# Kernel optimization log

Measured on AMD Instinct MI355X. Metric: run time of the kernel, lower is better.

## Reference

```python
import jax, jax.numpy as jnp
import numpy as np

NEG = -9e15
ALPHA = 0.2  # leaky-relu slope


def gat_layer(h, mask, W, a, concat):
    # h: [N, Fin], W: [Fin, Fout], a: [2*Fout, 1], mask: [N, N]
    Wh = h @ W                                   # [N, Fout]
    F = Wh.shape[1]
    e = jax.nn.leaky_relu(Wh @ a[:F] + (Wh @ a[F:]).T, ALPHA)  # [N, N]
    att = jax.nn.softmax(jnp.where(mask > 0, e, NEG), axis=1)
    out = att @ Wh                               # [N, Fout]
    return jax.nn.elu(out) if concat else out


def gat(x, mask, W, a, Wo, ao):
    # W: [H, Fin, Fhid], a: [H, 2*Fhid, 1]
    heads = jax.vmap(lambda Wi, ai: gat_layer(x, mask, Wi, ai, True))(W, a)  # [H, N, Fhid]
    h = jnp.transpose(heads, (1, 0, 2)).reshape(x.shape[0], -1)  # [N, H*Fhid] (concat dim=1)
    return jax.nn.elu(gat_layer(h, mask, Wo, ao, False))


def setup_inputs() -> dict:
    key = jax.random.key(0)
    ks = jax.random.split(key, 16)
    N, Fin, H, Fhid, Ffin, P = 4096, 256, 4, 64, 64, 16
    x = jax.random.normal(ks[0], (N, Fin), jnp.float32)
    eye = jnp.eye(N, dtype=jnp.float32)
    sadj = jnp.maximum((jax.random.uniform(ks[1], (N, N)) < 0.005).astype(jnp.float32), eye)
    sadj2 = jnp.maximum((jax.random.uniform(ks[2], (N, N)) < 0.005).astype(jnp.float32), eye)
    s = 0.1
    inp = {
        "x": x, "sadj": sadj, "sadj2": sadj2,
        "W1": s * jax.random.normal(ks[3], (H, Fin, Fhid), jnp.float32),
        "a1": s * jax.random.normal(ks[4], (H, 2 * Fhid, 1), jnp.float32),
        "Wo1": s * jax.random.normal(ks[5], (H * Fhid, Ffin), jnp.float32),
        "ao1": s * jax.random.normal(ks[6], (2 * Ffin, 1), jnp.float32),
        "W2": s * jax.random.normal(ks[7], (H, Fin, Fhid), jnp.float32),
        "a2": s * jax.random.normal(ks[8], (H, 2 * Fhid, 1), jnp.float32),
        "Wo2": s * jax.random.normal(ks[9], (H * Fhid, Ffin), jnp.float32),
        "ao2": s * jax.random.normal(ks[10], (2 * Ffin, 1), jnp.float32),
        "Wp1": s * jax.random.normal(ks[11], (Ffin, P), jnp.float32),
        "bp1": jnp.zeros((P,), jnp.float32),
        "Wp2": s * jax.random.normal(ks[12], (P, 1), jnp.float32),
    }
    return inp


def reference(x, sadj, sadj2, W1, a1, Wo1, ao1, W2, a2, Wo2, ao2, Wp1, bp1, Wp2):
    emb1 = gat(x, sadj, W1, a1, Wo1, ao1)    # [N, Ffin]
    emb2 = gat(x, sadj2, W2, a2, Wo2, ao2)   # [N, Ffin]
    emb = jnp.stack([emb1, emb2], axis=1)    # [N, 2, Ffin]
    w = jnp.tanh(emb @ Wp1 + bp1) @ Wp2      # [N, 2, 1]
    beta = jax.nn.softmax(w, axis=1)
    return jnp.sum(beta * emb, axis=1)       # [N, Ffin]
```

## Files before the change

### kernel.cpp

```cpp
#include <hip/hip_runtime.h>
#include <hip/hip_bf16.h>
#include <stdint.h>


typedef short short8 __attribute__((ext_vector_type(8)));
typedef __bf16 bf16x8 __attribute__((ext_vector_type(8)));
typedef float floatx4 __attribute__((ext_vector_type(4)));
typedef unsigned int uintx4 __attribute__((ext_vector_type(4)));

#define MAXDEG 128
#define LRELU 0.2f

template <typename V>
__device__ inline auto mfma_impl(V a, V b, floatx4 c, int)
    -> decltype(__builtin_amdgcn_mfma_f32_16x16x32_bf16(a, b, c, 0, 0, 0)) {
  return __builtin_amdgcn_mfma_f32_16x16x32_bf16(a, b, c, 0, 0, 0);
}
template <typename V>
__device__ inline floatx4 mfma_impl(V a, V b, floatx4 c, long) {
  return __builtin_amdgcn_mfma_f32_16x16x32_bf16(
      __builtin_bit_cast(bf16x8, a), __builtin_bit_cast(bf16x8, b), c, 0, 0, 0);
}
__device__ inline floatx4 MFMA16(short8 a, short8 b, floatx4 c) {
  return mfma_impl(a, b, c, 0);
}

__device__ inline bool is_bf16_inputs(const void* sadj) {
  return ((*(const uint32_t*)sadj) & 0xFFFFu) == 0x3F80u;
}
__device__ inline float ldval(const void* p, size_t i, bool isbf) {
  if (isbf) return __bfloat162float(((const __hip_bfloat16*)p)[i]);
  return ((const float*)p)[i];
}
__device__ inline uint16_t f2bf_bits(float f) {
  __hip_bfloat16 h = __float2bfloat16(f);
  return *(uint16_t*)&h;
}

static constexpr size_t OFF_ADJ = 0;
static constexpr size_t OFF_DEG = OFF_ADJ + (size_t)2 * 4096 * MAXDEG * 4;
static constexpr size_t OFF_XB  = OFF_DEG + (size_t)2 * 4096 * 4;
static constexpr size_t OFF_WT  = OFF_XB  + (size_t)4096 * 256 * 2;
static constexpr size_t OFF_WOT = OFF_WT  + (size_t)2 * 4 * 64 * 256 * 2;
static constexpr size_t OFF_AV  = OFF_WOT + (size_t)2 * 64 * 256 * 2;
static constexpr size_t OFF_AOV = OFF_AV  + (size_t)2 * 4 * 128 * 4;
static constexpr size_t OFF_WP1 = OFF_AOV + (size_t)2 * 128 * 4;
static constexpr size_t OFF_BP1 = OFF_WP1 + (size_t)64 * 16 * 4;
static constexpr size_t OFF_WP2 = OFF_BP1 + 64;
static constexpr size_t OFF_WH1 = OFF_WP2 + 192;
static constexpr size_t OFF_S1  = OFF_WH1 + (size_t)2 * 4096 * 256 * 4;
static constexpr size_t OFF_D1  = OFF_S1  + (size_t)2 * 4 * 4096 * 4;
static constexpr size_t OFF_H2  = OFF_D1  + (size_t)2 * 4 * 4096 * 4;
static constexpr size_t OFF_WH2 = OFF_H2  + (size_t)2 * 4096 * 256 * 2;
static constexpr size_t OFF_S2  = OFF_WH2 + (size_t)2 * 4096 * 64 * 4;
static constexpr size_t OFF_D2  = OFF_S2  + (size_t)2 * 4096 * 4;
static constexpr size_t OFF_EMB = OFF_D2  + (size_t)2 * 4096 * 4;
static constexpr size_t OFF_MB  = OFF_EMB + (size_t)2 * 4096 * 64 * 4;

__global__ __launch_bounds__(256) void k_conv(const void* x,
    const void* W1, const void* W2, const void* Wo1, const void* Wo2,
    const void* a1, const void* a2, const void* ao1, const void* ao2,
    const void* wp1, const void* bp1, const void* wp2, const void* sadj,
    uint16_t* xb, uint16_t* Wt, uint16_t* Wot,
    float* Av, float* Aov, float* Wp1v, float* Bp1v, float* Wp2v) {
  bool isbf = is_bf16_inputs(sadj);
  int bid = blockIdx.x;
  if (bid < 1024) {
    int i0 = (bid * 256 + threadIdx.x) * 4;
    if (isbf) {
      *(uint64_t*)(xb + i0) = *(const uint64_t*)((const uint16_t*)x + i0);
    } else {
      const float* xf = (const float*)x;
      float4 f = *(const float4*)(xf + i0);
      xb[i0 + 0] = f2bf_bits(f.x);
      xb[i0 + 1] = f2bf_bits(f.y);
      xb[i0 + 2] = f2bf_bits(f.z);
      xb[i0 + 3] = f2bf_bits(f.w);
    }
    return;
  }
  int idx = (bid - 1024) * 256 + threadIdx.x;
  if (idx < 131072) {
    int k = idx & 255, f = (idx >> 8) & 63, h = (idx >> 14) & 3, g = idx >> 16;
    const void* W = g ? W2 : W1;
    Wt[idx] = f2bf_bits(ldval(W, (size_t)h * 16384 + (size_t)k * 64 + f, isbf));
  } else if (idx < 163840) {
    int j = idx - 131072;
    int k = j & 255, f = (j >> 8) & 63, g = j >> 14;
    const void* W = g ? Wo2 : Wo1;
    Wot[j] = f2bf_bits(ldval(W, (size_t)k * 64 + f, isbf));
  } else if (idx < 166176) {
    int q = idx - 163840;
    if (q < 512)        Av[q] = ldval(a1, q, isbf);
    else if (q < 1024)  Av[q] = ldval(a2, q - 512, isbf);
    else if (q < 1152)  Aov[q - 1024] = ldval(ao1, q - 1024, isbf);
    else if (q < 1280)  Aov[q - 1152 + 128] = ldval(ao2, q - 1152, isbf);
    else if (q < 2304)  Wp1v[q - 1280] = ldval(wp1, q - 1280, isbf);
    else if (q < 2320)  Bp1v[q - 2304] = ldval(bp1, q - 2304, isbf);
    else                Wp2v[q - 2320] = ldval(wp2, q - 2320, isbf);
  }
}

__global__ __launch_bounds__(256) void k_scan(const void* sadj, const void* sadj2,
                                              uint8_t* mbytes) {
  bool isbf = is_bf16_inputs(sadj);
  int tid = blockIdx.x * blockDim.x + threadIdx.x;
  int nt = gridDim.x * blockDim.x;
  const int NCHUNK = 4194304;
  if (isbf) {
    const uint16_t* m0 = (const uint16_t*)sadj;
    const uint16_t* m1 = (const uint16_t*)sadj2;
    for (int c = tid; c < NCHUNK; c += nt) {
      const uint16_t* src = (c < 2097152) ? m0 : m1;
      int cc = c & 2097151;
      uintx4 v = __builtin_nontemporal_load((const uintx4*)src + cc);
      uint32_t wd[4] = {v.x, v.y, v.z, v.w};
      uint32_t byte = 0;
#pragma unroll
      for (int k = 0; k < 8; ++k) {
        uint16_t val = (uint16_t)(wd[k >> 1] >> ((k & 1) * 16));
        if (val != 0 && !(val & 0x8000)) byte |= 1u << k;
      }
      mbytes[c] = (uint8_t)byte;
    }
  } else {
    const float* m0 = (const float*)sadj;
    const float* m1 = (const float*)sadj2;
    for (int c = tid; c < NCHUNK; c += nt) {
      const float* src = (c < 2097152) ? m0 : m1;
      size_t cc = (size_t)(c & 2097151) * 8;
      floatx4 va = __builtin_nontemporal_load((const floatx4*)(src + cc));
      floatx4 vb = __builtin_nontemporal_load((const floatx4*)(src + cc + 4));
      float vals[8] = {va.x, va.y, va.z, va.w, vb.x, vb.y, vb.z, vb.w};
      uint32_t byte = 0;
#pragma unroll
      for (int k = 0; k < 8; ++k)
        if (vals[k] > 0.f) byte |= 1u << k;
      mbytes[c] = (uint8_t)byte;
    }
  }
}

__global__ __launch_bounds__(256) void k_compact(const uint8_t* mbytes,
                                                 int* adj, int* deg) {
  int w = blockIdx.x * 4 + (threadIdx.x >> 6);
  int lane = threadIdx.x & 63;
  uint64_t bits = *((const uint64_t*)(mbytes + (size_t)w * 512) + lane);
  int* out = adj + (size_t)w * MAXDEG;
  int c = __popcll(bits);
  int pre = c;
#pragma unroll
  for (int o = 1; o < 64; o <<= 1) {
    int tv = __shfl_up(pre, o);
    if (lane >= o) pre += tv;
  }
  int total = __shfl(pre, 63);
  int off = pre - c;
  int base = lane * 64;
  while (bits) {
    int i = __ffsll((unsigned long long)bits) - 1;
    bits &= bits - 1;
    if (off < MAXDEG) out[off] = base + i;
    ++off;
  }
  if (lane == 0) deg[w] = total < MAXDEG ? total : MAXDEG;
}

__global__ __launch_bounds__(256) void k_gemm1(const uint16_t* xb, const uint16_t* Wt,
                                               const float* Av,
                                               float* Wh1, float* s1, float* d1) {
  int w = blockIdx.x * 4 + (threadIdx.x >> 6);
  int lane = threadIdx.x & 63;
  int q = lane >> 4, c = lane & 15;
  int g = w >> 10, rem = w & 1023;
  int m0 = (rem >> 2) << 4, h = rem & 3;
  const uint16_t* B = Wt + (size_t)(g * 4 + h) * 64 * 256;
  floatx4 acc[4] = {};
  const uint16_t* arow = xb + (size_t)(m0 + c) * 256 + q * 8;
  for (int kk = 0; kk < 8; ++kk) {
    short8 a = *(const short8*)(arow + kk * 32);
#pragma unroll
    for (int t = 0; t < 4; ++t) {
      short8 b = *(const short8*)(B + (size_t)(t * 16 + c) * 256 + kk * 32 + q * 8);
      acc[t] = MFMA16(a, b, acc[t]);
    }
  }
  float* Crow = Wh1 + (size_t)(g * 4096 + m0) * 256 + h * 64;
#pragma unroll
  for (int t = 0; t < 4; ++t)
#pragma unroll
    for (int r = 0; r < 4; ++r)
      Crow[(size_t)(q * 4 + r) * 256 + t * 16 + c] = acc[t][r];
  const float* ag = Av + (g * 4 + h) * 128;
  float as[4], ad[4];
#pragma unroll
  for (int t = 0; t < 4; ++t) { as[t] = ag[t * 16 + c]; ad[t] = ag[64 + t * 16 + c]; }
#pragma unroll
  for (int r = 0; r < 4; ++r) {
    float ps = 0.f, pd = 0.f;
#pragma unroll
    for (int t = 0; t < 4; ++t) { ps += acc[t][r] * as[t]; pd += acc[t][r] * ad[t]; }
#pragma unroll
    for (int o = 1; o < 16; o <<= 1) { ps += __shfl_xor(ps, o); pd += __shfl_xor(pd, o); }
    if (c == 0) {
      int n = m0 + q * 4 + r;
      s1[((size_t)(g * 4096 + n)) * 4 + h] = ps;
      d1[((size_t)(g * 4096 + n)) * 4 + h] = pd;
    }
  }
}

__global__ __launch_bounds__(256) void k_gemm2(const uint16_t* h2, const uint16_t* Wot,
                                               const float* Aov,
                                               float* Wh2, float* s2, float* d2) {
  int w = blockIdx.x * 4 + (threadIdx.x >> 6);
  int lane = threadIdx.x & 63;
  int q = lane >> 4, c = lane & 15;
  int g = w >> 8, m0 = (w & 255) << 4;
  const uint16_t* A = h2 + (size_t)g * 4096 * 256;
  const uint16_t* B = Wot + (size_t)g * 64 * 256;
  floatx4 acc[4] = {};
  const uint16_t* arow = A + (size_t)(m0 + c) * 256 + q * 8;
  for (int kk = 0; kk < 8; ++kk) {
    short8 a = *(const short8*)(arow + kk * 32);
#pragma unroll
    for (int t = 0; t < 4; ++t) {
      short8 b = *(const short8*)(B + (size_t)(t * 16 + c) * 256 + kk * 32 + q * 8);
      acc[t] = MFMA16(a, b, acc[t]);
    }
  }
  float* Crow = Wh2 + (size_t)(g * 4096 + m0) * 64;
#pragma unroll
  for (int t = 0; t < 4; ++t)
#pragma unroll
    for (int r = 0; r < 4; ++r)
      Crow[(size_t)(q * 4 + r) * 64 + t * 16 + c] = acc[t][r];
  const float* ag = Aov + g * 128;
  float as[4], ad[4];
#pragma unroll
  for (int t = 0; t < 4; ++t) { as[t] = ag[t * 16 + c]; ad[t] = ag[64 + t * 16 + c]; }
#pragma unroll
  for (int r = 0; r < 4; ++r) {
    float ps = 0.f, pd = 0.f;
#pragma unroll
    for (int t = 0; t < 4; ++t) { ps += acc[t][r] * as[t]; pd += acc[t][r] * ad[t]; }
#pragma unroll
    for (int o = 1; o < 16; o <<= 1) { ps += __shfl_xor(ps, o); pd += __shfl_xor(pd, o); }
    if (c == 0) {
      int n = m0 + q * 4 + r;
      s2[g * 4096 + n] = ps;
      d2[g * 4096 + n] = pd;
    }
  }
}

__global__ __launch_bounds__(256) void k_att1(const int* adj, const int* deg,
    const float* s1, const float* d1, const float* Wh1, uint16_t* h2) {
  __shared__ float pbuf[4][4][MAXDEG];
  __shared__ int jbuf[4][MAXDEG];
  int wv = threadIdx.x >> 6, lane = threadIdx.x & 63;
  int w = blockIdx.x * 4 + wv;
  int g = w >> 12;
  int gn = w;
  int dg = deg[gn];
  const int* nbr = adj + (size_t)gn * MAXDEG;
  float4 s4 = *(const float4*)(s1 + (size_t)gn * 4);
  const float4* d4 = (const float4*)(d1) + (size_t)g * 4096;

  bool v0 = lane < dg, v1 = lane + 64 < dg;
  int j0 = 0, j1 = 0;
  if (v0) j0 = nbr[lane];
  if (v1) j1 = nbr[lane + 64];
  float4 dj0 = d4[j0];
  float4 dj1 = d4[j1];
  if (v0) jbuf[wv][lane] = j0;
  if (v1) jbuf[wv][lane + 64] = j1;

  const float ninf = -3.0e38f;
  float sa[4] = {s4.x, s4.y, s4.z, s4.w};
  float d0a[4] = {dj0.x, dj0.y, dj0.z, dj0.w};
  float d1a[4] = {dj1.x, dj1.y, dj1.z, dj1.w};
#pragma unroll
  for (int h = 0; h < 4; ++h) {
    float t0 = sa[h] + d0a[h]; t0 = t0 > 0.f ? t0 : LRELU * t0;
    float t1 = sa[h] + d1a[h]; t1 = t1 > 0.f ? t1 : LRELU * t1;
    float e0 = v0 ? t0 : ninf;
    float e1 = v1 ? t1 : ninf;
    float m = fmaxf(e0, e1);
#pragma unroll
    for (int o = 32; o; o >>= 1) m = fmaxf(m, __shfl_xor(m, o));
    float p0 = v0 ? __expf(e0 - m) : 0.f;
    float p1 = v1 ? __expf(e1 - m) : 0.f;
    float l = p0 + p1;
#pragma unroll
    for (int o = 32; o; o >>= 1) l += __shfl_xor(l, o);
    float inv = __frcp_rn(l);
    pbuf[wv][h][lane] = p0 * inv;
    pbuf[wv][h][lane + 64] = p1 * inv;
  }
  int myh = lane >> 4;
  const float* prow = pbuf[wv][myh];
  const int* jb = jbuf[wv];
  const float4* Wg = (const float4*)(Wh1) + (size_t)g * 4096 * 64;
  float ax = 0.f, ay = 0.f, az = 0.f, aw = 0.f;
  for (int i = 0; i < dg; i += 8) {
    float pv[8];
    float4 wv8[8];
#pragma unroll
    for (int k = 0; k < 8; ++k) {
      int idx = i + k;
      bool vv = idx < dg;
      int sidx = vv ? idx : 0;
      int j = jb[sidx];
      pv[k] = vv ? prow[sidx] : 0.f;
      wv8[k] = Wg[(size_t)j * 64 + lane];
    }
#pragma unroll
    for (int k = 0; k < 8; ++k) {
      ax += pv[k] * wv8[k].x;
      ay += pv[k] * wv8[k].y;
      az += pv[k] * wv8[k].z;
      aw += pv[k] * wv8[k].w;
    }
  }
  ax = ax > 0.f ? ax : __expf(ax) - 1.f;
  ay = ay > 0.f ? ay : __expf(ay) - 1.f;
  az = az > 0.f ? az : __expf(az) - 1.f;
  aw = aw > 0.f ? aw : __expf(aw) - 1.f;
  ushort4 o4 = {f2bf_bits(ax), f2bf_bits(ay), f2bf_bits(az), f2bf_bits(aw)};
  *(ushort4*)(h2 + (size_t)gn * 256 + lane * 4) = o4;
}

__global__ __launch_bounds__(256) void k_att2(const int* adj, const int* deg,
    const float* s2, const float* d2, const float* Wh2, float* emb) {
  __shared__ float pbuf[4][MAXDEG];
  __shared__ int jbuf[4][MAXDEG];
  int wv = threadIdx.x >> 6, lane = threadIdx.x & 63;
  int w = blockIdx.x * 4 + wv;
  int g = w >> 12;
  int gn = w;
  int dg = deg[gn];
  const int* nbr = adj + (size_t)gn * MAXDEG;
  float sn = s2[gn];
  const float* dp = d2 + (size_t)g * 4096;

  bool v0 = lane < dg, v1 = lane + 64 < dg;
  int j0 = 0, j1 = 0;
  if (v0) j0 = nbr[lane];
  if (v1) j1 = nbr[lane + 64];
  float dd0 = dp[j0], dd1 = dp[j1];
  if (v0) jbuf[wv][lane] = j0;
  if (v1) jbuf[wv][lane + 64] = j1;

  const float ninf = -3.0e38f;
  float t0 = sn + dd0; t0 = t0 > 0.f ? t0 : LRELU * t0;
  float t1 = sn + dd1; t1 = t1 > 0.f ? t1 : LRELU * t1;
  float e0 = v0 ? t0 : ninf;
  float e1 = v1 ? t1 : ninf;
  float m = fmaxf(e0, e1);
#pragma unroll
  for (int o = 32; o; o >>= 1) m = fmaxf(m, __shfl_xor(m, o));
  float p0 = v0 ? __expf(e0 - m) : 0.f;
  float p1 = v1 ? __expf(e1 - m) : 0.f;
  float l = p0 + p1;
#pragma unroll
  for (int o = 32; o; o >>= 1) l += __shfl_xor(l, o);
  float inv = __frcp_rn(l);
  pbuf[wv][lane] = p0 * inv;
  pbuf[wv][lane + 64] = p1 * inv;

  int mye = lane >> 4, c4 = lane & 15;
  const float4* Wg = (const float4*)(Wh2) + (size_t)g * 4096 * 16;
  float ax = 0.f, ay = 0.f, az = 0.f, aw = 0.f;
  for (int i = 0; i < dg; i += 8) {
    int ia = i + mye, ib = i + 4 + mye;
    bool va = ia < dg, vb = ib < dg;
    int sa_ = va ? ia : 0, sb_ = vb ? ib : 0;
    int ja = jbuf[wv][sa_], jb2 = jbuf[wv][sb_];
    float pa = va ? pbuf[wv][sa_] : 0.f;
    float pb = vb ? pbuf[wv][sb_] : 0.f;
    float4 wa = Wg[(size_t)ja * 16 + c4];
    float4 wb = Wg[(size_t)jb2 * 16 + c4];
    ax += pa * wa.x + pb * wb.x;
    ay += pa * wa.y + pb * wb.y;
    az += pa * wa.z + pb * wb.z;
    aw += pa * wa.w + pb * wb.w;
  }
#pragma unroll
  for (int o = 16; o <= 32; o <<= 1) {
    ax += __shfl_xor(ax, o);
    ay += __shfl_xor(ay, o);
    az += __shfl_xor(az, o);
    aw += __shfl_xor(aw, o);
  }
  if (lane < 16) {
    ax = ax > 0.f ? ax : __expf(ax) - 1.f;
    ay = ay > 0.f ? ay : __expf(ay) - 1.f;
    az = az > 0.f ? az : __expf(az) - 1.f;
    aw = aw > 0.f ? aw : __expf(aw) - 1.f;
    float4 r = {ax, ay, az, aw};
    *(float4*)(emb + (size_t)gn * 64 + lane * 4) = r;
  }
}

__global__ __launch_bounds__(256) void k_final(const float* emb, const float* Wp1v,
    const float* Bp1v, const float* Wp2v, const void* sadj, void* out) {
  __shared__ float se[4][128];
  __shared__ float st[4][32];
  __shared__ float sw[4][2];
  int wv = threadIdx.x >> 6, lane = threadIdx.x & 63;
  int n = blockIdx.x * 4 + wv;
  bool isbf = is_bf16_inputs(sadj);
  float e1 = emb[(size_t)n * 64 + lane];
  float e2 = emb[(size_t)(4096 + n) * 64 + lane];
  se[wv][lane] = e1;
  se[wv][64 + lane] = e2;
  __syncthreads();
  if (lane < 32) {
    int g = lane >> 4, p = lane & 15;
    float s = Bp1v[p];
    const float* eb = &se[wv][g * 64];
    for (int f = 0; f < 64; ++f) s += eb[f] * Wp1v[f * 16 + p];
    st[wv][lane] = tanhf(s);
  }
  __syncthreads();
  if (lane < 2) {
    float s = 0.f;
    for (int p = 0; p < 16; ++p) s += st[wv][lane * 16 + p] * Wp2v[p];
    sw[wv][lane] = s;
  }
  __syncthreads();
  float w0 = sw[wv][0], w1 = sw[wv][1];
  float mx = fmaxf(w0, w1);
  float p0 = __expf(w0 - mx), p1 = __expf(w1 - mx);
  float inv = 1.f / (p0 + p1);
  float v = (p0 * e1 + p1 * e2) * inv;
  if (isbf) ((uint16_t*)out)[(size_t)n * 64 + lane] = f2bf_bits(v);
  else ((float*)out)[(size_t)n * 64 + lane] = v;
}

extern "C" void kernel_launch(void* const* d_in, const int* in_sizes, int n_in,
                              void* d_out, int out_size, void* d_ws, size_t ws_size,
                              hipStream_t stream) {
  const void* x    = d_in[0];
  const void* sadj = d_in[1];
  const void* sadj2 = d_in[2];
  const void* W1  = d_in[3];
  const void* a1  = d_in[4];
  const void* Wo1 = d_in[5];
  const void* ao1 = d_in[6];
  const void* W2  = d_in[7];
  const void* a2  = d_in[8];
  const void* Wo2 = d_in[9];
  const void* ao2 = d_in[10];
  const void* Wp1 = d_in[11];
  const void* bp1 = d_in[12];
  const void* Wp2 = d_in[13];

  char* ws = (char*)d_ws;
  int* adj      = (int*)(ws + OFF_ADJ);
  int* deg      = (int*)(ws + OFF_DEG);
  uint16_t* xb  = (uint16_t*)(ws + OFF_XB);
  uint16_t* Wt  = (uint16_t*)(ws + OFF_WT);
  uint16_t* Wot = (uint16_t*)(ws + OFF_WOT);
  float* Av     = (float*)(ws + OFF_AV);
  float* Aov    = (float*)(ws + OFF_AOV);
  float* Wp1v   = (float*)(ws + OFF_WP1);
  float* Bp1v   = (float*)(ws + OFF_BP1);
  float* Wp2v   = (float*)(ws + OFF_WP2);
  float* Wh1    = (float*)(ws + OFF_WH1);
  float* s1     = (float*)(ws + OFF_S1);
  float* d1     = (float*)(ws + OFF_D1);
  uint16_t* h2  = (uint16_t*)(ws + OFF_H2);
  float* Wh2    = (float*)(ws + OFF_WH2);
  float* s2     = (float*)(ws + OFF_S2);
  float* d2     = (float*)(ws + OFF_D2);
  float* emb    = (float*)(ws + OFF_EMB);
  uint8_t* mb   = (uint8_t*)(ws + OFF_MB);

  k_scan<<<1024, 256, 0, stream>>>(sadj, sadj2, mb);
  k_conv<<<1680, 256, 0, stream>>>(x, W1, W2, Wo1, Wo2, a1, a2, ao1, ao2,
                                   Wp1, bp1, Wp2, sadj,
                                   xb, Wt, Wot, Av, Aov, Wp1v, Bp1v, Wp2v);
  k_compact<<<2048, 256, 0, stream>>>(mb, adj, deg);
  k_gemm1<<<512, 256, 0, stream>>>(xb, Wt, Av, Wh1, s1, d1);
  k_att1<<<2048, 256, 0, stream>>>(adj, deg, s1, d1, Wh1, h2);
  k_gemm2<<<128, 256, 0, stream>>>(h2, Wot, Aov, Wh2, s2, d2);
  k_att2<<<2048, 256, 0, stream>>>(adj, deg, s2, d2, Wh2, emb);
  k_final<<<1024, 256, 0, stream>>>(emb, Wp1v, Bp1v, Wp2v, sadj, d_out);
}
```

Baseline: 225.1 us.

## Merge scan/conv and compact/gemm1 kernels, store Wh in bf16, fuse final into att2

Combines the mask scan with input conversion, and the adjacency compaction with the first GEMM, so that independent work shares a launch and eight kernels drop to five. The intermediate Wh1 and Wh2 projections are now stored in bf16 instead of fp32, which halves the bytes moved by the neighbour gathers in the attention kernels. The semantic-attention combine is fused into att2, so per-node embeddings stay in shared memory and are never written to global memory. The mask scan also switches from nontemporal loads to plain loads. The trade-off is extra bf16 rounding of Wh and larger kernels with more divergent block roles.

```diff
diff --git a/kernel.cpp b/kernel.cpp
--- a/kernel.cpp
+++ b/kernel.cpp
@@ -35,6 +35,10 @@
 __device__ inline uint16_t f2bf_bits(float f) {
   __hip_bfloat16 h = __float2bfloat16(f);
   return *(uint16_t*)&h;
+}
+__device__ inline float bf2f(uint16_t u) {
+  uint32_t i = ((uint32_t)u) << 16;
+  return __builtin_bit_cast(float, i);
 }
 
 static constexpr size_t OFF_ADJ = 0;
@@ -47,26 +51,64 @@
 static constexpr size_t OFF_WP1 = OFF_AOV + (size_t)2 * 128 * 4;
 static constexpr size_t OFF_BP1 = OFF_WP1 + (size_t)64 * 16 * 4;
 static constexpr size_t OFF_WP2 = OFF_BP1 + 64;
-static constexpr size_t OFF_WH1 = OFF_WP2 + 192;
-static constexpr size_t OFF_S1  = OFF_WH1 + (size_t)2 * 4096 * 256 * 4;
+static constexpr size_t OFF_WH1B = OFF_WP2 + 192;
+static constexpr size_t OFF_S1  = OFF_WH1B + (size_t)2 * 4096 * 256 * 2;
 static constexpr size_t OFF_D1  = OFF_S1  + (size_t)2 * 4 * 4096 * 4;
 static constexpr size_t OFF_H2  = OFF_D1  + (size_t)2 * 4 * 4096 * 4;
-static constexpr size_t OFF_WH2 = OFF_H2  + (size_t)2 * 4096 * 256 * 2;
-static constexpr size_t OFF_S2  = OFF_WH2 + (size_t)2 * 4096 * 64 * 4;
+static constexpr size_t OFF_WH2B = OFF_H2 + (size_t)2 * 4096 * 256 * 2;
+static constexpr size_t OFF_S2  = OFF_WH2B + (size_t)2 * 4096 * 64 * 2;
 static constexpr size_t OFF_D2  = OFF_S2  + (size_t)2 * 4096 * 4;
-static constexpr size_t OFF_EMB = OFF_D2  + (size_t)2 * 4096 * 4;
-static constexpr size_t OFF_MB  = OFF_EMB + (size_t)2 * 4096 * 64 * 4;
-
-__global__ __launch_bounds__(256) void k_conv(const void* x,
+static constexpr size_t OFF_MB  = OFF_D2  + (size_t)2 * 4096 * 4;
+
+__global__ __launch_bounds__(256) void k_pre(const void* sadj, const void* sadj2,
+    const void* x,
     const void* W1, const void* W2, const void* Wo1, const void* Wo2,
     const void* a1, const void* a2, const void* ao1, const void* ao2,
-    const void* wp1, const void* bp1, const void* wp2, const void* sadj,
-    uint16_t* xb, uint16_t* Wt, uint16_t* Wot,
+    const void* wp1, const void* bp1, const void* wp2,
+    uint8_t* mbytes, uint16_t* xb, uint16_t* Wt, uint16_t* Wot,
     float* Av, float* Aov, float* Wp1v, float* Bp1v, float* Wp2v) {
   bool isbf = is_bf16_inputs(sadj);
   int bid = blockIdx.x;
-  if (bid < 1024) {
-    int i0 = (bid * 256 + threadIdx.x) * 4;
+  if (bid < 2048) {
+    int tid = bid * 256 + threadIdx.x;
+    int nt = 2048 * 256;
+    const int NCHUNK = 4194304;
+    if (isbf) {
+      const uint16_t* m0 = (const uint16_t*)sadj;
+      const uint16_t* m1 = (const uint16_t*)sadj2;
+      for (int c = tid; c < NCHUNK; c += nt) {
+        const uint16_t* src = (c < 2097152) ? m0 : m1;
+        int cc = c & 2097151;
+        uintx4 v = *((const uintx4*)src + cc);
+        uint32_t wd[4] = {v.x, v.y, v.z, v.w};
+        uint32_t byte = 0;
+#pragma unroll
+        for (int k = 0; k < 8; ++k) {
+          uint16_t val = (uint16_t)(wd[k >> 1] >> ((k & 1) * 16));
+          if (val != 0 && !(val & 0x8000)) byte |= 1u << k;
+        }
+        mbytes[c] = (uint8_t)byte;
+      }
+    } else {
+      const float* m0 = (const float*)sadj;
+      const float* m1 = (const float*)sadj2;
+      for (int c = tid; c < NCHUNK; c += nt) {
+        const float* src = (c < 2097152) ? m0 : m1;
+        size_t cc = (size_t)(c & 2097151) * 8;
+        floatx4 va = *(const floatx4*)(src + cc);
+        floatx4 vb = *(const floatx4*)(src + cc + 4);
+        float vals[8] = {va.x, va.y, va.z, va.w, vb.x, vb.y, vb.z, vb.w};
+        uint32_t byte = 0;
+#pragma unroll
+        for (int k = 0; k < 8; ++k)
+          if (vals[k] > 0.f) byte |= 1u << k;
+        mbytes[c] = (uint8_t)byte;
+      }
+    }
+    return;
+  }
+  if (bid < 3072) {
+    int i0 = ((bid - 2048) * 256 + threadIdx.x) * 4;
     if (isbf) {
       *(uint64_t*)(xb + i0) = *(const uint64_t*)((const uint16_t*)x + i0);
     } else {
@@ -79,7 +121,7 @@
     }
     return;
   }
-  int idx = (bid - 1024) * 256 + threadIdx.x;
+  int idx = (bid - 3072) * 256 + threadIdx.x;
   if (idx < 131072) {
     int k = idx & 255, f = (idx >> 8) & 63, h = (idx >> 14) & 3, g = idx >> 16;
     const void* W = g ? W2 : W1;
@@ -101,75 +143,35 @@
   }
 }
 
-__global__ __launch_bounds__(256) void k_scan(const void* sadj, const void* sadj2,
-                                              uint8_t* mbytes) {
-  bool isbf = is_bf16_inputs(sadj);
-  int tid = blockIdx.x * blockDim.x + threadIdx.x;
-  int nt = gridDim.x * blockDim.x;
-  const int NCHUNK = 4194304;
-  if (isbf) {
-    const uint16_t* m0 = (const uint16_t*)sadj;
-    const uint16_t* m1 = (const uint16_t*)sadj2;
-    for (int c = tid; c < NCHUNK; c += nt) {
-      const uint16_t* src = (c < 2097152) ? m0 : m1;
-      int cc = c & 2097151;
-      uintx4 v = __builtin_nontemporal_load((const uintx4*)src + cc);
-      uint32_t wd[4] = {v.x, v.y, v.z, v.w};
-      uint32_t byte = 0;
-#pragma unroll
-      for (int k = 0; k < 8; ++k) {
-        uint16_t val = (uint16_t)(wd[k >> 1] >> ((k & 1) * 16));
-        if (val != 0 && !(val & 0x8000)) byte |= 1u << k;
-      }
-      mbytes[c] = (uint8_t)byte;
-    }
-  } else {
-    const float* m0 = (const float*)sadj;
-    const float* m1 = (const float*)sadj2;
-    for (int c = tid; c < NCHUNK; c += nt) {
-      const float* src = (c < 2097152) ? m0 : m1;
-      size_t cc = (size_t)(c & 2097151) * 8;
-      floatx4 va = __builtin_nontemporal_load((const floatx4*)(src + cc));
-      floatx4 vb = __builtin_nontemporal_load((const floatx4*)(src + cc + 4));
-      float vals[8] = {va.x, va.y, va.z, va.w, vb.x, vb.y, vb.z, vb.w};
-      uint32_t byte = 0;
-#pragma unroll
-      for (int k = 0; k < 8; ++k)
-        if (vals[k] > 0.f) byte |= 1u << k;
-      mbytes[c] = (uint8_t)byte;
-    }
-  }
-}
-
-__global__ __launch_bounds__(256) void k_compact(const uint8_t* mbytes,
-                                                 int* adj, int* deg) {
-  int w = blockIdx.x * 4 + (threadIdx.x >> 6);
-  int lane = threadIdx.x & 63;
-  uint64_t bits = *((const uint64_t*)(mbytes + (size_t)w * 512) + lane);
-  int* out = adj + (size_t)w * MAXDEG;
-  int c = __popcll(bits);
-  int pre = c;
-#pragma unroll
-  for (int o = 1; o < 64; o <<= 1) {
-    int tv = __shfl_up(pre, o);
-    if (lane >= o) pre += tv;
-  }
-  int total = __shfl(pre, 63);
-  int off = pre - c;
-  int base = lane * 64;
-  while (bits) {
-    int i = __ffsll((unsigned long long)bits) - 1;
-    bits &= bits - 1;
-    if (off < MAXDEG) out[off] = base + i;
-    ++off;
-  }
-  if (lane == 0) deg[w] = total < MAXDEG ? total : MAXDEG;
-}
-
-__global__ __launch_bounds__(256) void k_gemm1(const uint16_t* xb, const uint16_t* Wt,
-                                               const float* Av,
-                                               float* Wh1, float* s1, float* d1) {
-  int w = blockIdx.x * 4 + (threadIdx.x >> 6);
+__global__ __launch_bounds__(256) void k_cg(const uint8_t* mbytes,
+    const uint16_t* xb, const uint16_t* Wt, const float* Av,
+    int* adj, int* deg, uint16_t* Wh1b, float* s1, float* d1) {
+  int bid = blockIdx.x;
+  if (bid < 2048) {
+    int w = bid * 4 + (threadIdx.x >> 6);
+    int lane = threadIdx.x & 63;
+    uint64_t bits = *((const uint64_t*)(mbytes + (size_t)w * 512) + lane);
+    int* out = adj + (size_t)w * MAXDEG;
+    int c = __popcll(bits);
+    int pre = c;
+#pragma unroll
+    for (int o = 1; o < 64; o <<= 1) {
+      int tv = __shfl_up(pre, o);
+      if (lane >= o) pre += tv;
+    }
+    int total = __shfl(pre, 63);
+    int off = pre - c;
+    int base = lane * 64;
+    while (bits) {
+      int i = __ffsll((unsigned long long)bits) - 1;
+      bits &= bits - 1;
+      if (off < MAXDEG) out[off] = base + i;
+      ++off;
+    }
+    if (lane == 0) deg[w] = total < MAXDEG ? total : MAXDEG;
+    return;
+  }
+  int w = (bid - 2048) * 4 + (threadIdx.x >> 6);
   int lane = threadIdx.x & 63;
   int q = lane >> 4, c = lane & 15;
   int g = w >> 10, rem = w & 1023;
@@ -185,12 +187,12 @@
       acc[t] = MFMA16(a, b, acc[t]);
     }
   }
-  float* Crow = Wh1 + (size_t)(g * 4096 + m0) * 256 + h * 64;
+  uint16_t* Crow = Wh1b + (size_t)(g * 4096 + m0) * 256 + h * 64;
 #pragma unroll
   for (int t = 0; t < 4; ++t)
 #pragma unroll
     for (int r = 0; r < 4; ++r)
-      Crow[(size_t)(q * 4 + r) * 256 + t * 16 + c] = acc[t][r];
+      Crow[(size_t)(q * 4 + r) * 256 + t * 16 + c] = f2bf_bits(acc[t][r]);
   const float* ag = Av + (g * 4 + h) * 128;
   float as[4], ad[4];
 #pragma unroll
@@ -210,9 +212,86 @@
   }
 }
 
+__global__ __launch_bounds__(256) void k_att1(const int* adj, const int* deg,
+    const float* s1, const float* d1, const uint16_t* Wh1b, uint16_t* h2) {
+  __shared__ float pbuf[4][4][MAXDEG];
+  __shared__ int jbuf[4][MAXDEG];
+  int wv = threadIdx.x >> 6, lane = threadIdx.x & 63;
+  int w = blockIdx.x * 4 + wv;
+  int g = w >> 12;
+  int gn = w;
+  int dg = deg[gn];
+  const int* nbr = adj + (size_t)gn * MAXDEG;
+  float4 s4 = *(const float4*)(s1 + (size_t)gn * 4);
+  const float4* d4 = (const float4*)(d1) + (size_t)g * 4096;
+
+  bool v0 = lane < dg, v1 = lane + 64 < dg;
+  int j0 = 0, j1 = 0;
+  if (v0) j0 = nbr[lane];
+  if (v1) j1 = nbr[lane + 64];
+  float4 dj0 = d4[j0];
+  float4 dj1 = d4[j1];
+  if (v0) jbuf[wv][lane] = j0;
+  if (v1) jbuf[wv][lane + 64] = j1;
+
+  const float ninf = -3.0e38f;
+  float sa[4] = {s4.x, s4.y, s4.z, s4.w};
+  float d0a[4] = {dj0.x, dj0.y, dj0.z, dj0.w};
+  float d1a[4] = {dj1.x, dj1.y, dj1.z, dj1.w};
+#pragma unroll
+  for (int h = 0; h < 4; ++h) {
+    float t0 = sa[h] + d0a[h]; t0 = t0 > 0.f ? t0 : LRELU * t0;
+    float t1 = sa[h] + d1a[h]; t1 = t1 > 0.f ? t1 : LRELU * t1;
+    float e0 = v0 ? t0 : ninf;
+    float e1 = v1 ? t1 : ninf;
+    float m = fmaxf(e0, e1);
+#pragma unroll
+    for (int o = 32; o; o >>= 1) m = fmaxf(m, __shfl_xor(m, o));
+    float p0 = v0 ? __expf(e0 - m) : 0.f;
+    float p1 = v1 ? __expf(e1 - m) : 0.f;
+    float l = p0 + p1;
+#pragma unroll
+    for (int o = 32; o; o >>= 1) l += __shfl_xor(l, o);
+    float inv = __frcp_rn(l);
+    pbuf[wv][h][lane] = p0 * inv;
+    pbuf[wv][h][lane + 64] = p1 * inv;
+  }
+  int myh = lane >> 4;
+  const float* prow = pbuf[wv][myh];
+  const int* jb = jbuf[wv];
+  const uint16_t* Wg = Wh1b + (size_t)g * 4096 * 256;
+  float ax = 0.f, ay = 0.f, az = 0.f, aw = 0.f;
+  for (int i = 0; i < dg; i += 8) {
+    float pv[8];
+    ushort4 wv8[8];
+#pragma unroll
+    for (int k = 0; k < 8; ++k) {
+      int idx = i + k;
+      bool vv = idx < dg;
+      int sidx = vv ? idx : 0;
+      int j = jb[sidx];
+      pv[k] = vv ? prow[sidx] : 0.f;
+      wv8[k] = *(const ushort4*)(Wg + (size_t)j * 256 + lane * 4);
+    }
+#pragma unroll
+    for (int k = 0; k < 8; ++k) {
+      ax += pv[k] * bf2f(wv8[k].x);
+      ay += pv[k] * bf2f(wv8[k].y);
+      az += pv[k] * bf2f(wv8[k].z);
+      aw += pv[k] * bf2f(wv8[k].w);
+    }
+  }
+  ax = ax > 0.f ? ax : __expf(ax) - 1.f;
+  ay = ay > 0.f ? ay : __expf(ay) - 1.f;
+  az = az > 0.f ? az : __expf(az) - 1.f;
+  aw = aw > 0.f ? aw : __expf(aw) - 1.f;
+  ushort4 o4 = {f2bf_bits(ax), f2bf_bits(ay), f2bf_bits(az), f2bf_bits(aw)};
+  *(ushort4*)(h2 + (size_t)gn * 256 + lane * 4) = o4;
+}
+
 __global__ __launch_bounds__(256) void k_gemm2(const uint16_t* h2, const uint16_t* Wot,
                                                const float* Aov,
-                                               float* Wh2, float* s2, float* d2) {
+                                               uint16_t* Wh2b, float* s2, float* d2) {
   int w = blockIdx.x * 4 + (threadIdx.x >> 6);
   int lane = threadIdx.x & 63;
   int q = lane >> 4, c = lane & 15;
@@ -229,12 +308,12 @@
       acc[t] = MFMA16(a, b, acc[t]);
     }
   }
-  float* Crow = Wh2 + (size_t)(g * 4096 + m0) * 64;
+  uint16_t* Crow = Wh2b + (size_t)(g * 4096 + m0) * 64;
 #pragma unroll
   for (int t = 0; t < 4; ++t)
 #pragma unroll
     for (int r = 0; r < 4; ++r)
-      Crow[(size_t)(q * 4 + r) * 64 + t * 16 + c] = acc[t][r];
+      Crow[(size_t)(q * 4 + r) * 64 + t * 16 + c] = f2bf_bits(acc[t][r]);
   const float* ag = Aov + g * 128;
   float as[4], ad[4];
 #pragma unroll
@@ -254,91 +333,19 @@
   }
 }
 
-__global__ __launch_bounds__(256) void k_att1(const int* adj, const int* deg,
-    const float* s1, const float* d1, const float* Wh1, uint16_t* h2) {
-  __shared__ float pbuf[4][4][MAXDEG];
-  __shared__ int jbuf[4][MAXDEG];
-  int wv = threadIdx.x >> 6, lane = threadIdx.x & 63;
-  int w = blockIdx.x * 4 + wv;
-  int g = w >> 12;
-  int gn = w;
-  int dg = deg[gn];
-  const int* nbr = adj + (size_t)gn * MAXDEG;
-  float4 s4 = *(const float4*)(s1 + (size_t)gn * 4);
-  const float4* d4 = (const float4*)(d1) + (size_t)g * 4096;
-
-  bool v0 = lane < dg, v1 = lane + 64 < dg;
-  int j0 = 0, j1 = 0;
-  if (v0) j0 = nbr[lane];
-  if (v1) j1 = nbr[lane + 64];
-  float4 dj0 = d4[j0];
-  float4 dj1 = d4[j1];
-  if (v0) jbuf[wv][lane] = j0;
-  if (v1) jbuf[wv][lane + 64] = j1;
-
-  const float ninf = -3.0e38f;
-  float sa[4] = {s4.x, s4.y, s4.z, s4.w};
-  float d0a[4] = {dj0.x, dj0.y, dj0.z, dj0.w};
-  float d1a[4] = {dj1.x, dj1.y, dj1.z, dj1.w};
-#pragma unroll
-  for (int h = 0; h < 4; ++h) {
-    float t0 = sa[h] + d0a[h]; t0 = t0 > 0.f ? t0 : LRELU * t0;
-    float t1 = sa[h] + d1a[h]; t1 = t1 > 0.f ? t1 : LRELU * t1;
-    float e0 = v0 ? t0 : ninf;
-    float e1 = v1 ? t1 : ninf;
-    float m = fmaxf(e0, e1);
-#pragma unroll
-    for (int o = 32; o; o >>= 1) m = fmaxf(m, __shfl_xor(m, o));
-    float p0 = v0 ? __expf(e0 - m) : 0.f;
-    float p1 = v1 ? __expf(e1 - m) : 0.f;
-    float l = p0 + p1;
-#pragma unroll
-    for (int o = 32; o; o >>= 1) l += __shfl_xor(l, o);
-    float inv = __frcp_rn(l);
-    pbuf[wv][h][lane] = p0 * inv;
-    pbuf[wv][h][lane + 64] = p1 * inv;
-  }
-  int myh = lane >> 4;
-  const float* prow = pbuf[wv][myh];
-  const int* jb = jbuf[wv];
-  const float4* Wg = (const float4*)(Wh1) + (size_t)g * 4096 * 64;
-  float ax = 0.f, ay = 0.f, az = 0.f, aw = 0.f;
-  for (int i = 0; i < dg; i += 8) {
-    float pv[8];
-    float4 wv8[8];
-#pragma unroll
-    for (int k = 0; k < 8; ++k) {
-      int idx = i + k;
-      bool vv = idx < dg;
-      int sidx = vv ? idx : 0;
-      int j = jb[sidx];
-      pv[k] = vv ? prow[sidx] : 0.f;
-      wv8[k] = Wg[(size_t)j * 64 + lane];
-    }
-#pragma unroll
-    for (int k = 0; k < 8; ++k) {
-      ax += pv[k] * wv8[k].x;
-      ay += pv[k] * wv8[k].y;
-      az += pv[k] * wv8[k].z;
-      aw += pv[k] * wv8[k].w;
-    }
-  }
-  ax = ax > 0.f ? ax : __expf(ax) - 1.f;
-  ay = ay > 0.f ? ay : __expf(ay) - 1.f;
-  az = az > 0.f ? az : __expf(az) - 1.f;
-  aw = aw > 0.f ? aw : __expf(aw) - 1.f;
-  ushort4 o4 = {f2bf_bits(ax), f2bf_bits(ay), f2bf_bits(az), f2bf_bits(aw)};
-  *(ushort4*)(h2 + (size_t)gn * 256 + lane * 4) = o4;
-}
-
-__global__ __launch_bounds__(256) void k_att2(const int* adj, const int* deg,
-    const float* s2, const float* d2, const float* Wh2, float* emb) {
+__global__ __launch_bounds__(256) void k_att2f(const int* adj, const int* deg,
+    const float* s2, const float* d2, const uint16_t* Wh2b,
+    const float* Wp1v, const float* Bp1v, const float* Wp2v,
+    const void* sadj, void* out) {
   __shared__ float pbuf[4][MAXDEG];
   __shared__ int jbuf[4][MAXDEG];
+  __shared__ float emb_s[4][64];
+  __shared__ float st_s[2][32];
+  __shared__ float sw_s[2][2];
   int wv = threadIdx.x >> 6, lane = threadIdx.x & 63;
-  int w = blockIdx.x * 4 + wv;
-  int g = w >> 12;
-  int gn = w;
+  int g = wv >> 1, nl = wv & 1;
+  int n = blockIdx.x * 2 + nl;
+  int gn = g * 4096 + n;
   int dg = deg[gn];
   const int* nbr = adj + (size_t)gn * MAXDEG;
   float sn = s2[gn];
@@ -370,7 +377,7 @@
   pbuf[wv][lane + 64] = p1 * inv;
 
   int mye = lane >> 4, c4 = lane & 15;
-  const float4* Wg = (const float4*)(Wh2) + (size_t)g * 4096 * 16;
+  const uint16_t* Wg = Wh2b + (size_t)g * 4096 * 64;
   float ax = 0.f, ay = 0.f, az = 0.f, aw = 0.f;
   for (int i = 0; i < dg; i += 8) {
     int ia = i + mye, ib = i + 4 + mye;
@@ -379,12 +386,12 @@
     int ja = jbuf[wv][sa_], jb2 = jbuf[wv][sb_];
     float pa = va ? pbuf[wv][sa_] : 0.f;
     float pb = vb ? pbuf[wv][sb_] : 0.f;
-    float4 wa = Wg[(size_t)ja * 16 + c4];
-    float4 wb = Wg[(size_t)jb2 * 16 + c4];
-    ax += pa * wa.x + pb * wb.x;
-    ay += pa * wa.y + pb * wb.y;
-    az += pa * wa.z + pb * wb.z;
-    aw += pa * wa.w + pb * wb.w;
+    ushort4 wa = *(const ushort4*)(Wg + (size_t)ja * 64 + c4 * 4);
+    ushort4 wb = *(const ushort4*)(Wg + (size_t)jb2 * 64 + c4 * 4);
+    ax += pa * bf2f(wa.x) + pb * bf2f(wb.x);
+    ay += pa * bf2f(wa.y) + pb * bf2f(wb.y);
+    az += pa * bf2f(wa.z) + pb * bf2f(wb.z);
+    aw += pa * bf2f(wa.w) + pb * bf2f(wb.w);
   }
 #pragma unroll
   for (int o = 16; o <= 32; o <<= 1) {
@@ -399,44 +406,32 @@
     az = az > 0.f ? az : __expf(az) - 1.f;
     aw = aw > 0.f ? aw : __expf(aw) - 1.f;
     float4 r = {ax, ay, az, aw};
-    *(float4*)(emb + (size_t)gn * 64 + lane * 4) = r;
-  }
-}
-
-__global__ __launch_bounds__(256) void k_final(const float* emb, const float* Wp1v,
-    const float* Bp1v, const float* Wp2v, const void* sadj, void* out) {
-  __shared__ float se[4][128];
-  __shared__ float st[4][32];
-  __shared__ float sw[4][2];
-  int wv = threadIdx.x >> 6, lane = threadIdx.x & 63;
-  int n = blockIdx.x * 4 + wv;
-  bool isbf = is_bf16_inputs(sadj);
-  float e1 = emb[(size_t)n * 64 + lane];
-  float e2 = emb[(size_t)(4096 + n) * 64 + lane];
-  se[wv][lane] = e1;
-  se[wv][64 + lane] = e2;
+    *(float4*)&emb_s[wv][c4 * 4] = r;
+  }
   __syncthreads();
-  if (lane < 32) {
-    int g = lane >> 4, p = lane & 15;
-    float s = Bp1v[p];
-    const float* eb = &se[wv][g * 64];
-    for (int f = 0; f < 64; ++f) s += eb[f] * Wp1v[f * 16 + p];
-    st[wv][lane] = tanhf(s);
-  }
-  __syncthreads();
-  if (lane < 2) {
-    float s = 0.f;
-    for (int p = 0; p < 16; ++p) s += st[wv][lane * 16 + p] * Wp2v[p];
-    sw[wv][lane] = s;
-  }
-  __syncthreads();
-  float w0 = sw[wv][0], w1 = sw[wv][1];
-  float mx = fmaxf(w0, w1);
-  float p0 = __expf(w0 - mx), p1 = __expf(w1 - mx);
-  float inv = 1.f / (p0 + p1);
-  float v = (p0 * e1 + p1 * e2) * inv;
-  if (isbf) ((uint16_t*)out)[(size_t)n * 64 + lane] = f2bf_bits(v);
-  else ((float*)out)[(size_t)n * 64 + lane] = v;
+  if (wv < 2) {
+    float e1v = emb_s[wv][lane];
+    float e2v = emb_s[2 + wv][lane];
+    if (lane < 32) {
+      int gg = lane >> 4, p = lane & 15;
+      float s = Bp1v[p];
+      const float* eb = emb_s[gg * 2 + wv];
+      for (int f = 0; f < 64; ++f) s += eb[f] * Wp1v[f * 16 + p];
+      st_s[wv][lane] = tanhf(s);
+    }
+    if (lane < 2) {
+      float s = 0.f;
+      for (int p = 0; p < 16; ++p) s += st_s[wv][lane * 16 + p] * Wp2v[p];
+      sw_s[wv][lane] = s;
+    }
+    float w0 = sw_s[wv][0], w1 = sw_s[wv][1];
+    float mx = fmaxf(w0, w1);
+    float q0 = __expf(w0 - mx), q1 = __expf(w1 - mx);
+    float qi = 1.f / (q0 + q1);
+    float v = (q0 * e1v + q1 * e2v) * qi;
+    if (is_bf16_inputs(sadj)) ((uint16_t*)out)[(size_t)n * 64 + lane] = f2bf_bits(v);
+    else ((float*)out)[(size_t)n * 64 + lane] = v;
+  }
 }
 
 extern "C" void kernel_launch(void* const* d_in, const int* in_sizes, int n_in,
@@ -468,24 +463,21 @@
   float* Wp1v   = (float*)(ws + OFF_WP1);
   float* Bp1v   = (float*)(ws + OFF_BP1);
   float* Wp2v   = (float*)(ws + OFF_WP2);
-  float* Wh1    = (float*)(ws + OFF_WH1);
+  uint16_t* Wh1b = (uint16_t*)(ws + OFF_WH1B);
   float* s1     = (float*)(ws + OFF_S1);
   float* d1     = (float*)(ws + OFF_D1);
   uint16_t* h2  = (uint16_t*)(ws + OFF_H2);
-  float* Wh2    = (float*)(ws + OFF_WH2);
+  uint16_t* Wh2b = (uint16_t*)(ws + OFF_WH2B);
   float* s2     = (float*)(ws + OFF_S2);
   float* d2     = (float*)(ws + OFF_D2);
-  float* emb    = (float*)(ws + OFF_EMB);
   uint8_t* mb   = (uint8_t*)(ws + OFF_MB);
 
-  k_scan<<<1024, 256, 0, stream>>>(sadj, sadj2, mb);
-  k_conv<<<1680, 256, 0, stream>>>(x, W1, W2, Wo1, Wo2, a1, a2, ao1, ao2,
-                                   Wp1, bp1, Wp2, sadj,
-                                   xb, Wt, Wot, Av, Aov, Wp1v, Bp1v, Wp2v);
-  k_compact<<<2048, 256, 0, stream>>>(mb, adj, deg);
-  k_gemm1<<<512, 256, 0, stream>>>(xb, Wt, Av, Wh1, s1, d1);
-  k_att1<<<2048, 256, 0, stream>>>(adj, deg, s1, d1, Wh1, h2);
-  k_gemm2<<<128, 256, 0, stream>>>(h2, Wot, Aov, Wh2, s2, d2);
-  k_att2<<<2048, 256, 0, stream>>>(adj, deg, s2, d2, Wh2, emb);
-  k_final<<<1024, 256, 0, stream>>>(emb, Wp1v, Bp1v, Wp2v, sadj, d_out);
-}
+  k_pre<<<3728, 256, 0, stream>>>(sadj, sadj2, x, W1, W2, Wo1, Wo2,
+                                  a1, a2, ao1, ao2, Wp1, bp1, Wp2,
+                                  mb, xb, Wt, Wot, Av, Aov, Wp1v, Bp1v, Wp2v);
+  k_cg<<<2560, 256, 0, stream>>>(mb, xb, Wt, Av, adj, deg, Wh1b, s1, d1);
+  k_att1<<<2048, 256, 0, stream>>>(adj, deg, s1, d1, Wh1b, h2);
+  k_gemm2<<<128, 256, 0, stream>>>(h2, Wot, Aov, Wh2b, s2, d2);
+  k_att2f<<<2048, 256, 0, stream>>>(adj, deg, s2, d2, Wh2b,
+                                    Wp1v, Bp1v, Wp2v, sadj, d_out);
+}
```

Measured after the change: 232.1 us. +3.1%, slower.
